# Kernel optimization log

Hardware: AMD Instinct MI355X
Metric: run time of the kernel (lower is better)

## Reference

```python
import jax, jax.numpy as jnp
import numpy as np

B, N, M, C, K = 4, 4096, 4096, 64, 32
RADIUS = 0.1
EPS = 1e-5


def setup_inputs() -> dict:
    key = jax.random.key(0)
    ks = jax.random.split(key, 32)
    inp = {
        "query_xyz": jax.random.uniform(ks[0], (B, N, 3), jnp.float32),
        "support_xyz": jax.random.uniform(ks[1], (B, M, 3), jnp.float32),
        "query_mask": jax.random.randint(ks[2], (B, N), 0, 2, jnp.int32),
        "support_mask": jax.random.randint(ks[3], (B, M), 0, 2, jnp.int32),
        "support_features": jax.random.normal(ks[4], (B, C, M), jnp.float32),
    }
    names = ["theta1", "theta2", "phi", "psi", "alpha", "gamma1", "gamma2"]
    in_ch = {"theta1": 3}
    for j, nm in enumerate(names):
        inp[f"W_{nm}"] = jax.random.normal(ks[5 + j], (C, in_ch.get(nm, C)), jnp.float32) * 0.05
        inp[f"b_{nm}"] = jax.random.normal(ks[12 + j], (C,), jnp.float32) * 0.05
    for j, nm in enumerate(["theta", "gamma"]):
        inp[f"g_{nm}"] = 1.0 + 0.1 * jax.random.normal(ks[19 + 2 * j], (C,), jnp.float32)
        inp[f"be_{nm}"] = 0.1 * jax.random.normal(ks[20 + 2 * j], (C,), jnp.float32)
        inp[f"rm_{nm}"] = jnp.zeros((C,), jnp.float32)
        inp[f"rv_{nm}"] = jnp.ones((C,), jnp.float32)
    return inp


def _conv(W, b, x):
    # 1x1 Conv2d: channelwise linear on [B, C_in, N, K]
    return jnp.einsum('oc,bcnk->bonk', W, x) + b[None, :, None, None]


def _bn(x, g, be, rm, rv):
    # BatchNorm2d, inference form with running stats
    inv = g / jnp.sqrt(rv + EPS)
    return x * inv[None, :, None, None] + (be - rm * inv)[None, :, None, None]


def _forward(query_xyz, support_xyz, query_mask, support_mask, support_features, P):
    Bq, Nq = query_xyz.shape[:2]
    # pairwise squared distances [B, N, M]; masked support pushed to +inf
    d2 = jnp.sum((query_xyz[:, :, None, :] - support_xyz[:, None, :, :]) ** 2, axis=-1)
    d2 = jnp.where(support_mask[:, None, :] > 0, d2, jnp.inf)
    # ball query as K-nearest-within-radius
    neg, idx = jax.lax.top_k(-d2, K)                    # idx: [B, N, K]
    nbr_mask = (-neg) <= RADIUS ** 2                    # valid-neighbor mask
    flat = idx.reshape(Bq, Nq * K)
    x_j = jnp.take_along_axis(support_features, flat[:, None, :], axis=2).reshape(Bq, -1, Nq, K)
    g_xyz = jnp.take_along_axis(support_xyz, flat[:, :, None], axis=1).reshape(Bq, Nq, K, 3)
    # normalize_xyz=True -> offsets divided by radius; layout [B, 3, N, K]
    pos = ((g_xyz - query_xyz[:, :, None, :]) / RADIUS).transpose(0, 3, 1, 2)
    # nearest-neighbor query for x_i [B, C, N]
    idx_nn = jnp.argmin(d2, axis=-1)
    x_i = jnp.take_along_axis(support_features, idx_nn[:, None, :], axis=2)
    # positional encoding delta
    delta = jax.nn.relu(_bn(_conv(P['W_theta2'], P['b_theta2'],
                                  _conv(P['W_theta1'], P['b_theta1'], pos)),
                            P['g_theta'], P['be_theta'], P['rm_theta'], P['rv_theta']))
    lin_i = _conv(P['W_phi'], P['b_phi'], x_i[..., None])   # [B,C,N,1], broadcast over K
    lin_j = _conv(P['W_psi'], P['b_psi'], x_j)
    rel = lin_i - lin_j + delta
    rel = jax.nn.relu(_bn(_conv(P['W_gamma2'], P['b_gamma2'],
                                _conv(P['W_gamma1'], P['b_gamma1'], rel)),
                          P['g_gamma'], P['be_gamma'], P['rm_gamma'], P['rv_gamma']))
    weights = jax.nn.softmax(rel, axis=-1)                   # softmax over neighbor axis
    feats = _conv(P['W_alpha'], P['b_alpha'], x_j) + delta
    fmask = nbr_mask.astype(feats.dtype) + (1.0 - query_mask.astype(feats.dtype))[:, :, None]
    feats = feats * fmask[:, None, :, :]
    return jnp.sum(weights * feats, axis=-1)                 # [B, C, N]


def reference(query_xyz, support_xyz, query_mask, support_mask, support_features,
              W_theta1, b_theta1, W_theta2, b_theta2, W_phi, b_phi, W_psi, b_psi,
              W_alpha, b_alpha, W_gamma1, b_gamma1, W_gamma2, b_gamma2,
              g_theta, be_theta, rm_theta, rv_theta, g_gamma, be_gamma, rm_gamma, rv_gamma):
    P = dict(locals())
    return _forward(query_xyz, support_xyz, query_mask, support_mask, support_features, P)
```

## Files before the change

kernel.cpp:

```cpp
#include <hip/hip_runtime.h>
#include <cstdint>
#include <cstddef>

#define NN 4096
#define MM 4096
#define CC 64
#define KK 32
#define INF_F __builtin_huge_valf()

#define SC 2304
#define CCAP 2560
#define NBUCK 256

typedef __bf16 bf16x8 __attribute__((ext_vector_type(8)));
typedef __bf16 bf16x4 __attribute__((ext_vector_type(4)));
typedef float f32x16 __attribute__((ext_vector_type(16)));

#define NFRAG 40
#define ASTRIDE 68
#define ESTRIDE 36

#define WFENCE() asm volatile("s_waitcnt lgkmcnt(0)" ::: "memory")


__device__ __forceinline__ f32x16 zero16() {
  f32x16 z;
#pragma unroll
  for (int i = 0; i < 16; ++i) z[i] = 0.0f;
  return z;
}

__device__ __forceinline__ void conv1g(const bf16x8* __restrict__ Wf, int conv, int lane,
                                       const bf16x8* B4, f32x16& a0, f32x16& a1) {
#pragma unroll
  for (int s = 0; s < 4; ++s) {
    const bf16x8 w0 = Wf[((conv * 2 + 0) * 4 + s) * 64 + lane];
    const bf16x8 w1 = Wf[((conv * 2 + 1) * 4 + s) * 64 + lane];
    a0 = __builtin_amdgcn_mfma_f32_32x32x16_bf16(w0, B4[s], a0, 0, 0, 0);
    a1 = __builtin_amdgcn_mfma_f32_32x32x16_bf16(w1, B4[s], a1, 0, 0, 0);
  }
}

__device__ __forceinline__ void sort64(float& v, int& i, int lane) {
#pragma unroll
  for (int k = 2; k <= 64; k <<= 1) {
#pragma unroll
    for (int j = k >> 1; j > 0; j >>= 1) {
      const float ov = __shfl_xor(v, j);
      const int oi = __shfl_xor(i, j);
      const bool up = ((lane & k) == 0);
      const bool lower = ((lane & j) == 0);
      const bool take = (up == lower) ? (ov < v) : (ov > v);
      if (take) { v = ov; i = oi; }
    }
  }
}

__device__ __forceinline__ void insert_cands(float vv, int ii, float& sv, int& si,
                                             float& cmax, int lane) {
  unsigned long long cand = __ballot(vv < cmax);
  while (cand) {
    const int src = __ffsll((unsigned long long)cand) - 1;
    cand &= cand - 1;
    const float dc = __shfl(vv, src);
    if (dc < cmax) {
      const int im = __shfl(ii, src);
      const float up_s = __shfl_up(sv, 1);
      const int up_i = __shfl_up(si, 1);
      const bool pg = sv > dc;
      const bool pgu = (lane > 0) && (up_s > dc);
      const float ns = pg ? (pgu ? up_s : dc) : sv;
      const int ni = pg ? (pgu ? up_i : im) : si;
      if (lane < 32) { sv = ns; si = ni; }
      cmax = __shfl(sv, 31);
    }
  }
}

__global__ void pt_setup(const float* __restrict__ sf, const float* __restrict__ sxyz,
                         const int* __restrict__ smask,
                         const float* __restrict__ Wpsi, const float* __restrict__ W2,
                         const float* __restrict__ Wg1, const float* __restrict__ Wg2,
                         const float* __restrict__ Wa, const float* __restrict__ Wphi,
                         const float* __restrict__ gT, const float* __restrict__ beT,
                         const float* __restrict__ rmT, const float* __restrict__ rvT,
                         const float* __restrict__ gG, const float* __restrict__ beG,
                         const float* __restrict__ rmG, const float* __restrict__ rvG,
                         const float* __restrict__ b2, const float* __restrict__ bg1,
                         const float* __restrict__ bg2, const float* __restrict__ ba,
                         __bf16* __restrict__ ftb, float4* __restrict__ sx4,
                         __bf16* __restrict__ Wpack, float* __restrict__ WphiT,
                         float4* __restrict__ eo, float4* __restrict__ bo,
                         int* __restrict__ cnt2) {
  const int blk = blockIdx.x;
  const int tid = threadIdx.x;

  if (blk < 256) {
    const int b = blk >> 6;
    const int m = ((blk & 63) << 6) + (tid & 63);
    const int cg = tid >> 6;
    float v[16];
#pragma unroll
    for (int j = 0; j < 16; ++j) v[j] = sf[((size_t)(b * CC + cg * 16 + j)) * MM + m];
    __bf16* db = ftb + ((size_t)(b * MM + m)) * CC + cg * 16;
    bf16x8 t0, t1;
#pragma unroll
    for (int j = 0; j < 8; ++j) { t0[j] = (__bf16)v[j]; t1[j] = (__bf16)v[8 + j]; }
    *(bf16x8*)db = t0;
    *(bf16x8*)(db + 8) = t1;
    if (cg == 0) {
      const size_t g = (size_t)(b * MM + m);
      sx4[g] = make_float4(sxyz[g * 3 + 0], sxyz[g * 3 + 1], sxyz[g * 3 + 2], 0.0f);
    }
    return;
  }

  if (blk < 320) {
    __shared__ int hcnt[NBUCK];
    const int sub = blk - 256;
    const int b = sub >> 4;
    const int s = sub & 15;
    hcnt[tid] = 0;
    __syncthreads();
    const int m = s * 256 + tid;
    const size_t g = (size_t)b * MM + m;
    if (smask[g] > 0) {
      int bk = (int)(sxyz[g * 3 + 0] * 256.0f);
      bk = min(max(bk, 0), NBUCK - 1);
      atomicAdd(&hcnt[bk], 1);
    }
    __syncthreads();
    cnt2[(b * 16 + s) * NBUCK + tid] = hcnt[tid];
    return;
  }

  const int t = (blk - 320) * 256 + tid;
  if (t < NFRAG * 64) {
    const int lane = t & 63;
    const int fi = t >> 6;
    const int s = fi & 3;
    const int mt = (fi >> 2) & 1;
    const int conv = fi >> 3;
    const float* W = conv == 0 ? Wpsi : conv == 1 ? W2 : conv == 2 ? Wg1 : conv == 3 ? Wg2 : Wa;
    const int m = mt * 32 + (lane & 31);
    const int k0 = s * 16 + (lane >> 5) * 8;
    bf16x8 vh;
#pragma unroll
    for (int j = 0; j < 8; ++j) vh[j] = (__bf16)W[m * CC + k0 + j];
    ((bf16x8*)Wpack)[fi * 64 + lane] = vh;
    return;
  }
  const int t2 = t - NFRAG * 64;
  if (t2 < CC * CC) {
    WphiT[t2] = Wphi[(t2 & 63) * CC + (t2 >> 6)];
    return;
  }
  const int o = t2 - CC * CC;
  if (o < CC) {
    const float invT = gT[o] / sqrtf(rvT[o] + 1e-5f);
    const float invG = gG[o] / sqrtf(rvG[o] + 1e-5f);
    eo[o] = make_float4(invT, beT[o] - rmT[o] * invT, invG, beG[o] - rmG[o] * invG);
    bo[o] = make_float4(b2[o], bg1[o], bg2[o], ba[o]);
  }
}

__global__ void pt_scan(int* __restrict__ cnt2, int* __restrict__ boffp,
                        float4* __restrict__ cpts) {
  __shared__ int wtot[4];
  const int b = blockIdx.x;
  const int tid = threadIdx.x;
  const int lane = tid & 63;
  const int w = tid >> 6;

  int c[16];
  int tot = 0;
#pragma unroll
  for (int s = 0; s < 16; ++s) {
    c[s] = cnt2[(b * 16 + s) * NBUCK + tid];
    tot += c[s];
  }
  int inc = tot;
#pragma unroll
  for (int off = 1; off < 64; off <<= 1) {
    const int o = __shfl_up(inc, off);
    if (lane >= off) inc += o;
  }
  if (lane == 63) wtot[w] = inc;
  __syncthreads();
  int excl = inc - tot;
#pragma unroll
  for (int i = 0; i < 4; ++i) excl += (i < w) ? wtot[i] : 0;
  boffp[b * 257 + tid] = excl;
  const int total = wtot[0] + wtot[1] + wtot[2] + wtot[3];
  if (tid == 0) boffp[b * 257 + 256] = total;
  int base = excl;
#pragma unroll
  for (int s = 0; s < 16; ++s) {
    cnt2[(b * 16 + s) * NBUCK + tid] = base;
    base += c[s];
  }
  float4* dst = cpts + (size_t)b * CCAP;
  for (int i = total + tid; i < SC; i += 256)
    dst[i] = make_float4(1e4f, 1e4f, 1e4f, __int_as_float(0));
}

__global__ void pt_scatter(const float* __restrict__ sxyz, const int* __restrict__ smask,
                           const int* __restrict__ cnt2, float4* __restrict__ cpts) {
  __shared__ int cur[NBUCK];
  const int b = blockIdx.x >> 4;
  const int s = blockIdx.x & 15;
  const int tid = threadIdx.x;
  cur[tid] = cnt2[(b * 16 + s) * NBUCK + tid];
  __syncthreads();
  const int m = s * 256 + tid;
  const size_t g = (size_t)b * MM + m;
  if (smask[g] > 0) {
    const float x = sxyz[g * 3 + 0];
    const float y = sxyz[g * 3 + 1];
    const float z = sxyz[g * 3 + 2];
    int bk = (int)(x * 256.0f);
    bk = min(max(bk, 0), NBUCK - 1);
    const int pos = atomicAdd(&cur[bk], 1);
    cpts[(size_t)b * CCAP + pos] = make_float4(x, y, z, __int_as_float(m));
  }
}

__global__ void pt_knn(const float* __restrict__ qxyz, const float4* __restrict__ cpts,
                       const int* __restrict__ boff, const __bf16* __restrict__ ftb,
                       const float* __restrict__ WphiT, const float* __restrict__ bphi,
                       const float* __restrict__ bpsi,
                       int* __restrict__ oidx, unsigned* __restrict__ ovalid,
                       float* __restrict__ lin) {
  const int lane = threadIdx.x & 63;
  const int qi = blockIdx.x * 4 + (threadIdx.x >> 6);
  const int b = qi >> 12;
  const float qx = qxyz[qi * 3 + 0];
  const float qy = qxyz[qi * 3 + 1];
  const float qz = qxyz[qi * 3 + 2];
  const float4* sb = cpts + (size_t)b * CCAP;
  const int* bo = boff + b * 257;
  const int cnt = bo[256];

  float R = 0.155f;
#pragma unroll
  for (int it = 0; it < 2; ++it) {
    const float cx = fminf(qx + R, 1.0f) - fmaxf(qx - R, 0.0f);
    const float cy = fminf(qy + R, 1.0f) - fmaxf(qy - R, 0.0f);
    const float cz = fminf(qz + R, 1.0f) - fmaxf(qz - R, 0.0f);
    const float n = fmaxf((float)cnt * 0.5235988f * cx * cy * cz, 1.0f);
    R *= __powf(48.0f / n, 0.33333333f);
  }
  R = fminf(fmaxf(R, 0.06f), 0.7f);

  const int lob = max((int)((qx - R) * 256.0f), 0);
  const int hib = min((int)((qx + R) * 256.0f), NBUCK - 1);
  const int r0 = bo[lob] >> 6;
  const int r1 = (bo[hib + 1] + 63) >> 6;

  float v0 = INF_F, v1 = INF_F, v2 = INF_F, v3 = INF_F;
  int i0 = 0, i1 = 0, i2 = 0, i3 = 0;
  int r = r0;
#pragma unroll 1
  for (; r + 4 <= r1; r += 4) {
    float4 P[4];
#pragma unroll
    for (int u = 0; u < 4; ++u) P[u] = sb[(r + u) * 64 + lane];
#pragma unroll
    for (int u = 0; u < 4; ++u) {
      const float dx = P[u].x - qx, dy = P[u].y - qy, dz = P[u].z - qz;
      const float d = dx * dx + dy * dy + dz * dz;
      const int m = __float_as_int(P[u].w);
      const bool c3 = d < v3, c2 = d < v2, c1 = d < v1, c0 = d < v0;
      v3 = c3 ? (c2 ? v2 : d) : v3;  i3 = c3 ? (c2 ? i2 : m) : i3;
      v2 = c2 ? (c1 ? v1 : d) : v2;  i2 = c2 ? (c1 ? i1 : m) : i2;
      v1 = c1 ? (c0 ? v0 : d) : v1;  i1 = c1 ? (c0 ? i0 : m) : i1;
      v0 = c0 ? d : v0;              i0 = c0 ? m : i0;
    }
  }
#pragma unroll 1
  for (; r < r1; ++r) {
    const float4 p = sb[r * 64 + lane];
    const float dx = p.x - qx, dy = p.y - qy, dz = p.z - qz;
    const float d = dx * dx + dy * dy + dz * dz;
    const int m = __float_as_int(p.w);
    const bool c3 = d < v3, c2 = d < v2, c1 = d < v1, c0 = d < v0;
    v3 = c3 ? (c2 ? v2 : d) : v3;  i3 = c3 ? (c2 ? i2 : m) : i3;
    v2 = c2 ? (c1 ? v1 : d) : v2;  i2 = c2 ? (c1 ? i1 : m) : i2;
    v1 = c1 ? (c0 ? v0 : d) : v1;  i1 = c1 ? (c0 ? i0 : m) : i1;
    v0 = c0 ? d : v0;              i0 = c0 ? m : i0;
  }

  float sv = v0;
  int si = i0;
  sort64(sv, si, lane);
  float cmax = __shfl(sv, 31);
  insert_cands(v1, i1, sv, si, cmax, lane);
  insert_cands(v2, i2, sv, si, cmax, lane);
  insert_cands(v3, i3, sv, si, cmax, lane);

  if (__ballot(v3 < cmax) && r1 > r0) {
    {
      const float4 p = sb[r0 * 64 + lane];
      const float dx = p.x - qx, dy = p.y - qy, dz = p.z - qz;
      float v = dx * dx + dy * dy + dz * dz;
      int id = __float_as_int(p.w);
      sort64(v, id, lane);
      sv = v; si = id;
    }
    cmax = __shfl(sv, 31);
    for (int rr = r0 + 1; rr < r1; ++rr) {
      const float4 p = sb[rr * 64 + lane];
      const float dx = p.x - qx, dy = p.y - qy, dz = p.z - qz;
      const float d = dx * dx + dy * dy + dz * dz;
      insert_cands(d, __float_as_int(p.w), sv, si, cmax, lane);
    }
  }

  const float gl = (lob > 0) ? (qx - (float)lob * 0.00390625f) : INF_F;
  const float gr = (hib < NBUCK - 1) ? ((float)(hib + 1) * 0.00390625f - qx) : INF_F;
  const float G = fminf(gl, gr);
  if (cmax > G * G) {
    const float R1 = sqrtf(cmax);
    const int lob2 = max((int)((qx - R1) * 256.0f), 0);
    const int hib2 = min((int)((qx + R1) * 256.0f), NBUCK - 1);
    const int s0 = bo[lob2] >> 6;
    const int s1 = (bo[hib2 + 1] + 63) >> 6;
    for (int rr = s0; rr < r0; ++rr) {
      const float4 p = sb[rr * 64 + lane];
      const float dx = p.x - qx, dy = p.y - qy, dz = p.z - qz;
      insert_cands(dx * dx + dy * dy + dz * dz, __float_as_int(p.w), sv, si, cmax, lane);
    }
    for (int rr = r1; rr < s1; ++rr) {
      const float4 p = sb[rr * 64 + lane];
      const float dx = p.x - qx, dy = p.y - qy, dz = p.z - qz;
      insert_cands(dx * dx + dy * dy + dz * dz, __float_as_int(p.w), sv, si, cmax, lane);
    }
  }

  if (lane < 32) oidx[(size_t)qi * KK + lane] = si;
  const unsigned long long vb = __ballot((lane < 32) && (sv <= 0.01f));
  if (lane == 0) ovalid[qi] = (unsigned)(vb & 0xffffffffull);

  const int nnb = __shfl(si, 0);
  const bf16x8* xr = (const bf16x8*)(ftb + ((size_t)(b * MM + nnb)) * CC);
  float a = bphi[lane] - bpsi[lane];
#pragma unroll
  for (int i = 0; i < 8; ++i) {
    const bf16x8 xv = xr[i];
#pragma unroll
    for (int j = 0; j < 8; ++j) a += WphiT[(8 * i + j) * CC + lane] * (float)xv[j];
  }
  lin[qi * CC + lane] = a;
}

__launch_bounds__(256, 4)
__global__ void pt_fused(
    const float* __restrict__ qxyz, const float4* __restrict__ sx4,
    const int* __restrict__ qmask, const __bf16* __restrict__ ftb,
    const int* __restrict__ kidx, const unsigned* __restrict__ kvalid,
    const float* __restrict__ lin,
    const float* __restrict__ W1, const float* __restrict__ b1,
    const __bf16* __restrict__ Wpack, const float4* __restrict__ eo,
    const float4* __restrict__ bo, float* __restrict__ out) {
  __shared__ float EPI[4][CC * ESTRIDE];
  __shared__ float4 sEO[CC], sBO[CC];
  const int wid = threadIdx.x >> 6;
  const int lane = threadIdx.x & 63;
  const int g = lane >> 5;
  const int col = lane & 31;
  const int q = blockIdx.x * 4 + wid;
  const int b = q >> 12;
  const int nq = q & (NN - 1);
  float* epi = EPI[wid];
  __bf16* act = (__bf16*)epi;
  const bf16x8* Wf = (const bf16x8*)Wpack;

  sEO[lane] = eo[lane];
  sBO[lane] = bo[lane];
  WFENCE();

  const int idx = kidx[q * KK + col];
  const float fm = (float)((kvalid[q] >> col) & 1u) + 1.0f - (float)qmask[q];
  const __bf16* ftq = ftb + ((size_t)(b * MM + idx)) * CC;

  bf16x8 Xb[4];
#pragma unroll
  for (int s = 0; s < 4; ++s) Xb[s] = *(const bf16x8*)(ftq + s * 16 + g * 8);

  bf16x8 Tb[4];
  {
    const float qx = qxyz[q * 3 + 0], qy = qxyz[q * 3 + 1], qz = qxyz[q * 3 + 2];
    const float4 pj = sx4[(size_t)b * MM + idx];
    const float p0 = (pj.x - qx) * 10.0f;
    const float p1 = (pj.y - qy) * 10.0f;
    const float p2 = (pj.z - qz) * 10.0f;
#pragma unroll
    for (int s = 0; s < 4; ++s) {
      bf16x8 t;
#pragma unroll
      for (int j = 0; j < 8; ++j) {
        const int c = s * 16 + g * 8 + j;
        t[j] = (__bf16)(b1[c] + W1[c * 3 + 0] * p0 + W1[c * 3 + 1] * p1 + W1[c * 3 + 2] * p2);
      }
      Tb[s] = t;
    }
  }

  float DELv[32];
  {
    f32x16 aT0 = zero16(), aT1 = zero16();
    conv1g(Wf, 1, lane, Tb, aT0, aT1);
#pragma unroll
    for (int mt = 0; mt < 2; ++mt)
#pragma unroll
      for (int t = 0; t < 4; ++t)
#pragma unroll
        for (int i = 0; i < 4; ++i) {
          const int r = t * 4 + i;
          const int o = mt * 32 + 8 * t + 4 * g + i;
          const float4 e = sEO[o];
          DELv[mt * 16 + r] = fmaxf(((mt ? aT1[r] : aT0[r]) + sBO[o].x) * e.x + e.y, 0.0f);
        }
  }

  {
    f32x16 aP0 = zero16(), aP1 = zero16();
    conv1g(Wf, 0, lane, Xb, aP0, aP1);
#pragma unroll
    for (int mt = 0; mt < 2; ++mt)
#pragma unroll
      for (int t = 0; t < 4; ++t) {
        const int ob = mt * 32 + 8 * t + 4 * g;
        const float4 lv = *(const float4*)(lin + q * CC + ob);
        const float lva[4] = {lv.x, lv.y, lv.z, lv.w};
        bf16x4 w;
#pragma unroll
        for (int i = 0; i < 4; ++i) {
          const int r = t * 4 + i;
          w[i] = (__bf16)(lva[i] - (mt ? aP1[r] : aP0[r]) + DELv[mt * 16 + r]);
        }
        *(bf16x4*)(act + col * ASTRIDE + ob) = w;
      }
  }
  WFENCE();

  {
    bf16x8 Rb[4];
#pragma unroll
    for (int s = 0; s < 4; ++s) {
      const bf16x4 lo = *(const bf16x4*)(act + col * ASTRIDE + s * 16 + g * 8);
      const bf16x4 hi = *(const bf16x4*)(act + col * ASTRIDE + s * 16 + g * 8 + 4);
      Rb[s] = bf16x8{lo[0], lo[1], lo[2], lo[3], hi[0], hi[1], hi[2], hi[3]};
    }
    f32x16 a0 = zero16(), a1 = zero16();
    conv1g(Wf, 2, lane, Rb, a0, a1);
#pragma unroll
    for (int mt = 0; mt < 2; ++mt)
#pragma unroll
      for (int t = 0; t < 4; ++t) {
        const int ob = mt * 32 + 8 * t + 4 * g;
        bf16x4 w;
#pragma unroll
        for (int i = 0; i < 4; ++i) {
          const int r = t * 4 + i;
          w[i] = (__bf16)((mt ? a1[r] : a0[r]) + sBO[ob + i].y);
        }
        *(bf16x4*)(act + col * ASTRIDE + ob) = w;
      }
  }
  WFENCE();

  f32x16 h0 = zero16(), h1 = zero16();
  {
    bf16x8 Rb[4];
#pragma unroll
    for (int s = 0; s < 4; ++s) {
      const bf16x4 lo = *(const bf16x4*)(act + col * ASTRIDE + s * 16 + g * 8);
      const bf16x4 hi = *(const bf16x4*)(act + col * ASTRIDE + s * 16 + g * 8 + 4);
      Rb[s] = bf16x8{lo[0], lo[1], lo[2], lo[3], hi[0], hi[1], hi[2], hi[3]};
    }
    conv1g(Wf, 3, lane, Rb, h0, h1);
  }
  WFENCE();

#pragma unroll
  for (int mt = 0; mt < 2; ++mt)
#pragma unroll
    for (int t = 0; t < 4; ++t)
#pragma unroll
      for (int i = 0; i < 4; ++i) {
        const int r = t * 4 + i;
        const int o = mt * 32 + 4 * g + 8 * t + i;
        const float4 e = sEO[o];
        const float v = fmaxf(((mt ? h1[r] : h0[r]) + sBO[o].z) * e.z + e.w, 0.0f);
        epi[o * ESTRIDE + col] = v;
      }

  bf16x8 Xb2[4];
#pragma unroll
  for (int s = 0; s < 4; ++s) Xb2[s] = *(const bf16x8*)(ftq + s * 16 + g * 8);
  WFENCE();

  float ev[32];
  float sum;
  {
    const float* row = epi + lane * ESTRIDE;
    float mx = -INF_F;
#pragma unroll
    for (int n = 0; n < 32; n += 4) {
      const float4 t = *(const float4*)(row + n);
      ev[n] = t.x; ev[n + 1] = t.y; ev[n + 2] = t.z; ev[n + 3] = t.w;
      mx = fmaxf(mx, fmaxf(fmaxf(t.x, t.y), fmaxf(t.z, t.w)));
    }
    sum = 0.0f;
#pragma unroll
    for (int n = 0; n < 32; ++n) { ev[n] = __expf(ev[n] - mx); sum += ev[n]; }
  }
  WFENCE();

  f32x16 fa0 = zero16(), fa1 = zero16();
  conv1g(Wf, 4, lane, Xb2, fa0, fa1);

#pragma unroll
  for (int mt = 0; mt < 2; ++mt)
#pragma unroll
    for (int t = 0; t < 4; ++t)
#pragma unroll
      for (int i = 0; i < 4; ++i) {
        const int r = t * 4 + i;
        const int o = mt * 32 + 4 * g + 8 * t + i;
        const float f = ((mt ? fa1[r] : fa0[r]) + sBO[o].w + DELv[mt * 16 + r]) * fm;
        epi[o * ESTRIDE + col] = f;
      }
  WFENCE();

  {
    const float* row = epi + lane * ESTRIDE;
    float acc = 0.0f;
#pragma unroll
    for (int n = 0; n < 32; n += 4) {
      const float4 t = *(const float4*)(row + n);
      acc += ev[n] * t.x + ev[n + 1] * t.y + ev[n + 2] * t.z + ev[n + 3] * t.w;
    }
    out[((size_t)(b * CC + lane)) * NN + nq] = acc * __builtin_amdgcn_rcpf(sum);
  }
}

extern "C" void kernel_launch(void* const* d_in, const int* in_sizes, int n_in,
                              void* d_out, int out_size, void* d_ws, size_t ws_size,
                              hipStream_t stream) {
  (void)in_sizes; (void)n_in; (void)out_size; (void)ws_size;
  const float* qxyz = (const float*)d_in[0];
  const float* sxyz = (const float*)d_in[1];
  const int* qmask = (const int*)d_in[2];
  const int* smask = (const int*)d_in[3];
  const float* sfeat = (const float*)d_in[4];
  const float* W1 = (const float*)d_in[5];
  const float* b1 = (const float*)d_in[6];
  const float* W2 = (const float*)d_in[7];
  const float* b2 = (const float*)d_in[8];
  const float* Wphi = (const float*)d_in[9];
  const float* bphi = (const float*)d_in[10];
  const float* Wpsi = (const float*)d_in[11];
  const float* bpsi = (const float*)d_in[12];
  const float* Wa = (const float*)d_in[13];
  const float* ba = (const float*)d_in[14];
  const float* Wg1 = (const float*)d_in[15];
  const float* bg1 = (const float*)d_in[16];
  const float* Wg2 = (const float*)d_in[17];
  const float* bg2 = (const float*)d_in[18];
  const float* gT = (const float*)d_in[19];
  const float* beT = (const float*)d_in[20];
  const float* rmT = (const float*)d_in[21];
  const float* rvT = (const float*)d_in[22];
  const float* gG = (const float*)d_in[23];
  const float* beG = (const float*)d_in[24];
  const float* rmG = (const float*)d_in[25];
  const float* rvG = (const float*)d_in[26];

  char* ws = (char*)d_ws;
  int* kidx      = (int*)(ws + 0);
  unsigned* kval = (unsigned*)(ws + 2097152);
  __bf16* ftb    = (__bf16*)(ws + 2162688);
  float4* sx4    = (float4*)(ws + 4259840);
  float* lin     = (float*)(ws + 4521984);
  __bf16* Wpack  = (__bf16*)(ws + 8716288);
  float4* eo     = (float4*)(ws + 8757248);
  float4* bo     = (float4*)(ws + 8758272);
  float4* cpts   = (float4*)(ws + 8759296);
  float* WphiT   = (float*)(ws + 8923136);
  int* boffp     = (int*)(ws + 8939520);
  int* cnt2      = (int*)(ws + 8943744);

  hipLaunchKernelGGL(pt_setup, dim3(347), dim3(256), 0, stream,
                     sfeat, sxyz, smask,
                     Wpsi, W2, Wg1, Wg2, Wa, Wphi,
                     gT, beT, rmT, rvT, gG, beG, rmG, rvG, b2, bg1, bg2, ba,
                     ftb, sx4, Wpack, WphiT, eo, bo, cnt2);
  hipLaunchKernelGGL(pt_scan, dim3(4), dim3(256), 0, stream, cnt2, boffp, cpts);
  hipLaunchKernelGGL(pt_scatter, dim3(64), dim3(256), 0, stream, sxyz, smask, cnt2, cpts);
  hipLaunchKernelGGL(pt_knn, dim3(4096), dim3(256), 0, stream,
                     qxyz, cpts, boffp, ftb, WphiT, bphi, bpsi, kidx, kval, lin);
  hipLaunchKernelGGL(pt_fused, dim3(4096), dim3(256), 0, stream,
                     qxyz, sx4, qmask, ftb, kidx, kval, lin,
                     W1, b1, Wpack, eo, bo, (float*)d_out);
}
```

Before: 248.4 us.

## Fold bucket scan into scatter kernel and keep neighbor features in registers

Removes the separate pt_scan launch: each scatter block now recomputes the per-batch prefix sums over its bucket counts and derives its own slice offset, with designated blocks writing boffp and padding cpts. In pt_fused, the neighbor feature vectors are loaded once and kept live instead of being reloaded from global memory before the alpha conv. Launch bounds are relaxed from 4 to 3 blocks per CU to make room for the extra registers. This trades one kernel launch and a global reload for redundant scan work in every scatter block and possibly lower occupancy in the fused kernel.

```diff
diff --git a/kernel.cpp b/kernel.cpp
--- a/kernel.cpp
+++ b/kernel.cpp
@@ -164,10 +164,13 @@
   }
 }
 
-__global__ void pt_scan(int* __restrict__ cnt2, int* __restrict__ boffp,
-                        float4* __restrict__ cpts) {
+__global__ void pt_scatter(const float* __restrict__ sxyz, const int* __restrict__ smask,
+                           const int* __restrict__ cnt2, float4* __restrict__ cpts,
+                           int* __restrict__ boffp) {
+  __shared__ int cur[NBUCK];
   __shared__ int wtot[4];
-  const int b = blockIdx.x;
+  const int b = blockIdx.x >> 4;
+  const int s = blockIdx.x & 15;
   const int tid = threadIdx.x;
   const int lane = tid & 63;
   const int w = tid >> 6;
@@ -175,9 +178,9 @@
   int c[16];
   int tot = 0;
 #pragma unroll
-  for (int s = 0; s < 16; ++s) {
-    c[s] = cnt2[(b * 16 + s) * NBUCK + tid];
-    tot += c[s];
+  for (int ss = 0; ss < 16; ++ss) {
+    c[ss] = cnt2[(b * 16 + ss) * NBUCK + tid];
+    tot += c[ss];
   }
   int inc = tot;
 #pragma unroll
@@ -190,27 +193,20 @@
   int excl = inc - tot;
 #pragma unroll
   for (int i = 0; i < 4; ++i) excl += (i < w) ? wtot[i] : 0;
-  boffp[b * 257 + tid] = excl;
   const int total = wtot[0] + wtot[1] + wtot[2] + wtot[3];
-  if (tid == 0) boffp[b * 257 + 256] = total;
   int base = excl;
 #pragma unroll
-  for (int s = 0; s < 16; ++s) {
-    cnt2[(b * 16 + s) * NBUCK + tid] = base;
-    base += c[s];
-  }
-  float4* dst = cpts + (size_t)b * CCAP;
-  for (int i = total + tid; i < SC; i += 256)
-    dst[i] = make_float4(1e4f, 1e4f, 1e4f, __int_as_float(0));
-}
-
-__global__ void pt_scatter(const float* __restrict__ sxyz, const int* __restrict__ smask,
-                           const int* __restrict__ cnt2, float4* __restrict__ cpts) {
-  __shared__ int cur[NBUCK];
-  const int b = blockIdx.x >> 4;
-  const int s = blockIdx.x & 15;
-  const int tid = threadIdx.x;
-  cur[tid] = cnt2[(b * 16 + s) * NBUCK + tid];
+  for (int ss = 0; ss < 16; ++ss) base += (ss < s) ? c[ss] : 0;
+  cur[tid] = base;
+  if (s == 0) {
+    boffp[b * 257 + tid] = excl;
+    if (tid == 0) boffp[b * 257 + 256] = total;
+  }
+  if (s == 15) {
+    float4* dst = cpts + (size_t)b * CCAP;
+    for (int i = total + tid; i < SC; i += 256)
+      dst[i] = make_float4(1e4f, 1e4f, 1e4f, __int_as_float(0));
+  }
   __syncthreads();
   const int m = s * 256 + tid;
   const size_t g = (size_t)b * MM + m;
@@ -353,7 +349,7 @@
   lin[qi * CC + lane] = a;
 }
 
-__launch_bounds__(256, 4)
+__launch_bounds__(256, 3)
 __global__ void pt_fused(
     const float* __restrict__ qxyz, const float4* __restrict__ sx4,
     const int* __restrict__ qmask, const __bf16* __restrict__ ftb,
@@ -377,15 +373,16 @@
 
   sEO[lane] = eo[lane];
   sBO[lane] = bo[lane];
-  WFENCE();
 
   const int idx = kidx[q * KK + col];
   const float fm = (float)((kvalid[q] >> col) & 1u) + 1.0f - (float)qmask[q];
-  const __bf16* ftq = ftb + ((size_t)(b * MM + idx)) * CC;
 
   bf16x8 Xb[4];
-#pragma unroll
-  for (int s = 0; s < 4; ++s) Xb[s] = *(const bf16x8*)(ftq + s * 16 + g * 8);
+  {
+    const __bf16* ftq = ftb + ((size_t)(b * MM + idx)) * CC;
+#pragma unroll
+    for (int s = 0; s < 4; ++s) Xb[s] = *(const bf16x8*)(ftq + s * 16 + g * 8);
+  }
 
   bf16x8 Tb[4];
   {
@@ -405,6 +402,7 @@
       Tb[s] = t;
     }
   }
+  WFENCE();
 
   float DELv[32];
   {
@@ -495,10 +493,6 @@
         const float v = fmaxf(((mt ? h1[r] : h0[r]) + sBO[o].z) * e.z + e.w, 0.0f);
         epi[o * ESTRIDE + col] = v;
       }
-
-  bf16x8 Xb2[4];
-#pragma unroll
-  for (int s = 0; s < 4; ++s) Xb2[s] = *(const bf16x8*)(ftq + s * 16 + g * 8);
   WFENCE();
 
   float ev[32];
@@ -519,7 +513,7 @@
   WFENCE();
 
   f32x16 fa0 = zero16(), fa1 = zero16();
-  conv1g(Wf, 4, lane, Xb2, fa0, fa1);
+  conv1g(Wf, 4, lane, Xb, fa0, fa1);
 
 #pragma unroll
   for (int mt = 0; mt < 2; ++mt)
@@ -597,8 +591,8 @@
                      Wpsi, W2, Wg1, Wg2, Wa, Wphi,
                      gT, beT, rmT, rvT, gG, beG, rmG, rvG, b2, bg1, bg2, ba,
                      ftb, sx4, Wpack, WphiT, eo, bo, cnt2);
-  hipLaunchKernelGGL(pt_scan, dim3(4), dim3(256), 0, stream, cnt2, boffp, cpts);
-  hipLaunchKernelGGL(pt_scatter, dim3(64), dim3(256), 0, stream, sxyz, smask, cnt2, cpts);
+  hipLaunchKernelGGL(pt_scatter, dim3(64), dim3(256), 0, stream,
+                     sxyz, smask, cnt2, cpts, boffp);
   hipLaunchKernelGGL(pt_knn, dim3(4096), dim3(256), 0, stream,
                      qxyz, cpts, boffp, ftb, WphiT, bphi, bpsi, kidx, kval, lin);
   hipLaunchKernelGGL(pt_fused, dim3(4096), dim3(256), 0, stream,
```

Result: faster. 228.8 us (-7.9%).
